# Optimization experiments

Measured on AMD Instinct MI355X. Metric: run time of the kernel, lower is better.

Reference implementation:

```python
import jax, jax.numpy as jnp
import numpy as np

HOPS = 3  # matches init kwarg hops=3


def setup_inputs() -> dict:
    key = jax.random.key(0)
    k1, k2, k3, k4 = jax.random.split(key, 4)
    B, N, D, K = 4, 8192, 128, 32
    x = jax.random.normal(k1, (B, N, D), dtype=jnp.float32)
    knn_idx = jax.random.randint(k2, (B, N, K), 0, N)
    # nn.Linear(dim, 3*dim, bias=False): y = x @ W_qkv  (W stored as (D, 3D))
    W_qkv = jax.random.normal(k3, (D, 3 * D), dtype=jnp.float32) / np.sqrt(D)
    # nn.Linear(dim, dim) with bias
    W_out = jax.random.normal(k4, (D, D), dtype=jnp.float32) / np.sqrt(D)
    b_out = jnp.zeros((D,), dtype=jnp.float32)
    return {"x": x, "knn_idx": knn_idx, "W_qkv": W_qkv, "W_out": W_out, "b_out": b_out}


def reference(x, knn_idx, W_qkv, W_out, b_out):
    B, N, D = x.shape
    K = knn_idx.shape[-1]
    qkv = x @ W_qkv                      # [B,N,3D]
    q, kf, vf = jnp.split(qkv, 3, axis=-1)
    b_ids = jnp.arange(B)[:, None, None]  # broadcast with knn_idx -> (B,N,K)
    denom = K + 1e-6

    def diffuse(f):
        # adj @ f: out[knn_idx[b,n,j]] += f[b,n]; duplicates coalesce-sum.
        return jnp.zeros_like(f).at[b_ids, knn_idx].add(f[:, :, None, :]) / denom

    for _ in range(HOPS):
        vf = diffuse(vf)
        kf = diffuse(kf)

    attn = jnp.sum(q * kf, axis=-1, keepdims=True)  # [B,N,1]
    return (attn * vf) @ W_out + b_out
```

## Files before the change

### kernel.cpp

```cpp
#include <hip/hip_runtime.h>
#include <hip/hip_fp16.h>

#define BB     4
#define NN     8192
#define DD     128
#define KNN    32
#define BN     (BB*NN)
#define NK     (NN*KNN)
#define RPB    64
#define RROWS  128
#define RCAP   4608
#define NRANGE (BB*RPB)
#define SCAP   4608
#define BCAP   48

typedef _Float16 half8 __attribute__((ext_vector_type(8)));
typedef float f32x4 __attribute__((ext_vector_type(4)));

static __device__ __forceinline__ float inv_denom() { return 1.0f / 32.000001f; }

__global__ void compute_bmat(const float* __restrict__ Wqkv,
                             const float* __restrict__ Wout,
                             _Float16* __restrict__ BT16,
                             int* __restrict__ gcursor) {
    int e = blockIdx.x;
    int j = threadIdx.x;
    if (e == 0) gcursor[j] = 0;
    float acc = 0.f;
    if (j < DD) {
        int c = j;
        #pragma unroll 4
        for (int d = 0; d < DD; ++d)
            acc += Wqkv[c*3*DD + d] * Wqkv[e*3*DD + DD + d];
    } else {
        int o = j - DD;
        #pragma unroll 4
        for (int d = 0; d < DD; ++d)
            acc += Wqkv[e*3*DD + 2*DD + d] * Wout[d*DD + o];
    }
    BT16[(size_t)j*DD + e] = (_Float16)acc;
}

__global__ __launch_bounds__(256) void cast16_kernel(const float* __restrict__ in,
                                                     __half* __restrict__ out16) {
    int t = blockIdx.x * 256 + threadIdx.x;
    const float4* p = reinterpret_cast<const float4*>(in) + (size_t)t*2;
    float4 a = p[0], b = p[1];
    uint4 w;
    w.x = __builtin_bit_cast(unsigned, __floats2half2_rn(a.x, a.y));
    w.y = __builtin_bit_cast(unsigned, __floats2half2_rn(a.z, a.w));
    w.z = __builtin_bit_cast(unsigned, __floats2half2_rn(b.x, b.y));
    w.w = __builtin_bit_cast(unsigned, __floats2half2_rn(b.z, b.w));
    *(reinterpret_cast<uint4*>(out16) + t) = w;
}

__global__ __launch_bounds__(256) void partition_kernel(
        const int* __restrict__ idx,
        int* __restrict__ staging,
        int* __restrict__ gcursor) {
    __shared__ int bucket[RPB][BCAP];
    __shared__ int bcnt[RPB];
    __shared__ int gbase[RPB];

    int t  = threadIdx.x;
    int bb = blockIdx.x;
    int batch = bb >> 8;
    int c = bb & 255;
    if (t < RPB) bcnt[t] = 0;
    __syncthreads();

    int4 v = reinterpret_cast<const int4*>(idx)[batch*(NK/4) + c*256 + t];
    int nrow = (c*256 + t) >> 3;
    int mm[4] = {v.x, v.y, v.z, v.w};
    #pragma unroll
    for (int j = 0; j < 4; ++j) {
        int m = mm[j];
        int r = m >> 7;
        int p = atomicAdd(&bcnt[r], 1);
        if (p < BCAP) bucket[r][p] = ((m & 127) << 13) | nrow;
    }
    __syncthreads();

    if (t < RPB) {
        int n = min(bcnt[t], BCAP);
        bcnt[t] = n;
        gbase[t] = atomicAdd(&gcursor[batch*RPB + t], n);
    }
    __syncthreads();

    for (int u = t; u < RPB*BCAP; u += 256) {
        int k = u / BCAP, s = u % BCAP;
        if (s < bcnt[k])
            staging[(size_t)(batch*RPB + k)*SCAP + gbase[k] + s] = bucket[k][s];
    }
}

__global__ __launch_bounds__(512) void bin_kernel(
        const int* __restrict__ staging,
        const int* __restrict__ gcursor,
        unsigned short* __restrict__ srcs16,
        int* __restrict__ meta) {
    __shared__ unsigned short binned[RCAP];
    __shared__ int hist[RROWS], pfx[RROWS], cur[RROWS];

    int t  = threadIdx.x;
    int rg = blockIdx.x;
    int cnt = gcursor[rg];
    if (cnt > SCAP) cnt = SCAP;
    const int* sp = staging + (size_t)rg*SCAP;

    if (t < RROWS) { hist[t] = 0; cur[t] = 0; }
    __syncthreads();

    for (int u = t; u < cnt; u += 512)
        atomicAdd(&hist[sp[u] >> 13], 1);
    __syncthreads();

    if (t < 64) {
        int a = hist[2*t], b = hist[2*t+1];
        int s = a + b;
        #pragma unroll
        for (int d = 1; d < 64; d <<= 1) {
            int v = __shfl_up(s, d, 64);
            if (t >= d) s += v;
        }
        int excl = s - (a + b);
        pfx[2*t]   = excl;
        pfx[2*t+1] = excl + a;
    }
    __syncthreads();

    for (int u = t; u < cnt; u += 512) {
        int e = sp[u];
        int ml = e >> 13;
        int p = atomicAdd(&cur[ml], 1);
        binned[pfx[ml] + p] = (unsigned short)(e & 8191);
    }
    __syncthreads();

    int base = rg * RCAP;
    for (int u = t; u < cnt; u += 512) srcs16[base + u] = binned[u];
    if (t < RROWS) {
        int grow = (rg >> 6)*NN + (rg & 63)*RROWS + t;
        meta[grow] = ((base + pfx[t]) << 8) | min(hist[t], 255);
    }
}

__global__ __launch_bounds__(256) void hop_kernel(
        const __half* __restrict__ fin, __half* __restrict__ fout,
        const int* __restrict__ meta,
        const unsigned short* __restrict__ srcs16) {
    int i = blockIdx.x;
    int xcd = i & 7;
    int batch = xcd >> 1;
    int j = ((i >> 3) << 1) | (xcd & 1);
    int wave = threadIdx.x >> 6;
    int lane = threadIdx.x & 63;
    int h = lane >> 4;
    int l16 = lane & 15;
    int g0 = batch*NN + j*8 + wave*2;

    int mt0 = meta[g0], mt1 = meta[g0 + 1];
    int off0 = mt0 >> 8, cnt0 = mt0 & 255;
    int off1 = mt1 >> 8, cnt1 = mt1 & 255;
    const unsigned short* sp0 = srcs16 + off0;
    const unsigned short* sp1 = srcs16 + off1;
    const __half* fbatch = fin + (size_t)batch*NN*DD;
    int laneoff = l16*8;

    int sA[8], sB[8];
    #pragma unroll
    for (int u = 0; u < 8; ++u) {
        int a = sp0[h + 4*u]; sA[u] = (a > NN-1) ? 0 : a;
        int b = sp1[h + 4*u]; sB[u] = (b > NN-1) ? 0 : b;
    }
    uint4 vA[8], vB[8];
    #pragma unroll
    for (int u = 0; u < 8; ++u)
        vA[u] = *reinterpret_cast<const uint4*>(fbatch + (size_t)sA[u]*DD + laneoff);
    #pragma unroll
    for (int u = 0; u < 8; ++u)
        vB[u] = *reinterpret_cast<const uint4*>(fbatch + (size_t)sB[u]*DD + laneoff);

    float acc0[8] = {0,0,0,0,0,0,0,0};
    float acc1[8] = {0,0,0,0,0,0,0,0};
    auto accum = [](float* acc, const uint4& v, float m) {
        float2 f0 = __half22float2(__builtin_bit_cast(__half2, v.x));
        float2 f1 = __half22float2(__builtin_bit_cast(__half2, v.y));
        float2 f2 = __half22float2(__builtin_bit_cast(__half2, v.z));
        float2 f3 = __half22float2(__builtin_bit_cast(__half2, v.w));
        acc[0] = fmaf(f0.x, m, acc[0]); acc[1] = fmaf(f0.y, m, acc[1]);
        acc[2] = fmaf(f1.x, m, acc[2]); acc[3] = fmaf(f1.y, m, acc[3]);
        acc[4] = fmaf(f2.x, m, acc[4]); acc[5] = fmaf(f2.y, m, acc[5]);
        acc[6] = fmaf(f3.x, m, acc[6]); acc[7] = fmaf(f3.y, m, acc[7]);
    };
    #pragma unroll
    for (int u = 0; u < 8; ++u) {
        accum(acc0, vA[u], (h + 4*u < cnt0) ? 1.f : 0.f);
        accum(acc1, vB[u], (h + 4*u < cnt1) ? 1.f : 0.f);
    }

    if (cnt0 > 32) {
        uint4 v2[4]; int s2[4];
        #pragma unroll
        for (int u = 0; u < 4; ++u) {
            int s = sp0[32 + h + 4*u]; s2[u] = (s > NN-1) ? 0 : s;
        }
        #pragma unroll
        for (int u = 0; u < 4; ++u)
            v2[u] = *reinterpret_cast<const uint4*>(fbatch + (size_t)s2[u]*DD + laneoff);
        #pragma unroll
        for (int u = 0; u < 4; ++u)
            accum(acc0, v2[u], (32 + h + 4*u < cnt0) ? 1.f : 0.f);
        for (int e = 48 + h; e < cnt0; e += 4) {
            int s = sp0[e];
            uint4 v = *reinterpret_cast<const uint4*>(fbatch + (size_t)s*DD + laneoff);
            accum(acc0, v, 1.f);
        }
    }
    if (cnt1 > 32) {
        uint4 v2[4]; int s2[4];
        #pragma unroll
        for (int u = 0; u < 4; ++u) {
            int s = sp1[32 + h + 4*u]; s2[u] = (s > NN-1) ? 0 : s;
        }
        #pragma unroll
        for (int u = 0; u < 4; ++u)
            v2[u] = *reinterpret_cast<const uint4*>(fbatch + (size_t)s2[u]*DD + laneoff);
        #pragma unroll
        for (int u = 0; u < 4; ++u)
            accum(acc1, v2[u], (32 + h + 4*u < cnt1) ? 1.f : 0.f);
        for (int e = 48 + h; e < cnt1; e += 4) {
            int s = sp1[e];
            uint4 v = *reinterpret_cast<const uint4*>(fbatch + (size_t)s*DD + laneoff);
            accum(acc1, v, 1.f);
        }
    }

    #pragma unroll
    for (int q = 0; q < 8; ++q) {
        acc0[q] += __shfl_xor(acc0[q], 16);
        acc0[q] += __shfl_xor(acc0[q], 32);
        acc1[q] += __shfl_xor(acc1[q], 16);
        acc1[q] += __shfl_xor(acc1[q], 32);
    }

    const float s = inv_denom();
    if (h == 0) {
        uint4 w;
        w.x = __builtin_bit_cast(unsigned, __floats2half2_rn(acc0[0]*s, acc0[1]*s));
        w.y = __builtin_bit_cast(unsigned, __floats2half2_rn(acc0[2]*s, acc0[3]*s));
        w.z = __builtin_bit_cast(unsigned, __floats2half2_rn(acc0[4]*s, acc0[5]*s));
        w.w = __builtin_bit_cast(unsigned, __floats2half2_rn(acc0[6]*s, acc0[7]*s));
        *reinterpret_cast<uint4*>(fout + (size_t)g0*DD + laneoff) = w;
    } else if (h == 1) {
        uint4 w;
        w.x = __builtin_bit_cast(unsigned, __floats2half2_rn(acc1[0]*s, acc1[1]*s));
        w.y = __builtin_bit_cast(unsigned, __floats2half2_rn(acc1[2]*s, acc1[3]*s));
        w.z = __builtin_bit_cast(unsigned, __floats2half2_rn(acc1[4]*s, acc1[5]*s));
        w.w = __builtin_bit_cast(unsigned, __floats2half2_rn(acc1[6]*s, acc1[7]*s));
        *reinterpret_cast<uint4*>(fout + (size_t)(g0+1)*DD + laneoff) = w;
    }
}

__global__ __launch_bounds__(256) void final_mfma(
        const __half* __restrict__ x3h, const float* __restrict__ x,
        const _Float16* __restrict__ BT16, const float* __restrict__ bout,
        float* __restrict__ out) {
    __shared__ float attn_l[2][16];
    int t = threadIdx.x;
    int w = t >> 6;
    int lane = t & 63;
    int role = w & 1;
    int rh = w >> 1;
    int row0 = blockIdx.x * 32 + rh * 16;
    int lr = lane & 15;
    int lg = lane >> 4;

    const _Float16* x3p = reinterpret_cast<const _Float16*>(x3h);

    half8 a[4];
    #pragma unroll
    for (int kc = 0; kc < 4; ++kc)
        a[kc] = *reinterpret_cast<const half8*>(
            x3p + (size_t)(row0 + lr)*DD + kc*32 + lg*8);

    f32x4 acc[8];
    #pragma unroll
    for (int ti = 0; ti < 8; ++ti) {
        acc[ti] = (f32x4){0.f, 0.f, 0.f, 0.f};
        int col = role*128 + ti*16 + lr;
        const _Float16* bp = BT16 + (size_t)col*DD + lg*8;
        #pragma unroll
        for (int kc = 0; kc < 4; ++kc) {
            half8 b = *reinterpret_cast<const half8*>(bp + kc*32);
            acc[ti] = __builtin_amdgcn_mfma_f32_16x16x32_f16(a[kc], b, acc[ti], 0, 0, 0);
        }
    }

    if (role == 0) {
        #pragma unroll
        for (int reg = 0; reg < 4; ++reg) {
            int row = row0 + lg*4 + reg;
            const float* xr = x + (size_t)row*DD;
            float p = 0.f;
            #pragma unroll
            for (int ti = 0; ti < 8; ++ti)
                p = fmaf(acc[ti][reg], xr[ti*16 + lr], p);
            p += __shfl_xor(p, 1); p += __shfl_xor(p, 2);
            p += __shfl_xor(p, 4); p += __shfl_xor(p, 8);
            if (lr == 0) attn_l[rh][lg*4 + reg] = p;
        }
    }
    __syncthreads();
    if (role == 1) {
        #pragma unroll
        for (int reg = 0; reg < 4; ++reg) {
            int row = row0 + lg*4 + reg;
            float at = attn_l[rh][lg*4 + reg];
            float* orow = out + (size_t)row*DD;
            #pragma unroll
            for (int ti = 0; ti < 8; ++ti) {
                int col = ti*16 + lr;
                orow[col] = fmaf(at, acc[ti][reg], bout[col]);
            }
        }
    }
}

extern "C" void kernel_launch(void* const* d_in, const int* in_sizes, int n_in,
                              void* d_out, int out_size, void* d_ws, size_t ws_size,
                              hipStream_t stream) {
    const float* x    = (const float*)d_in[0];
    const int*   idx  = (const int*)  d_in[1];
    const float* Wqkv = (const float*)d_in[2];
    const float* Wout = (const float*)d_in[3];
    const float* bout = (const float*)d_in[4];
    float* out = (float*)d_out;

    char* ws = (char*)d_ws;
    __half*         x16     = (__half*)(ws);
    __half*         fa16    = (__half*)(ws + 8388608);
    __half*         fb16    = (__half*)(ws + 16777216);
    unsigned short* srcs16  = (unsigned short*)(ws + 25165824);
    int*            meta    = (int*)(ws + 27525376);
    _Float16*       BT16    = (_Float16*)(ws + 27656448);
    int*            staging = (int*)(ws + 27787520);
    int*            gcursor = (int*)(ws + 32506112);

    compute_bmat<<<DD, 256, 0, stream>>>(Wqkv, Wout, BT16, gcursor);
    cast16_kernel<<<BN*DD/8/256, 256, 0, stream>>>(x, x16);
    partition_kernel<<<1024, 256, 0, stream>>>(idx, staging, gcursor);
    bin_kernel<<<NRANGE, 512, 0, stream>>>(staging, gcursor, srcs16, meta);

    hop_kernel<<<4096, 256, 0, stream>>>(x16,  fa16, meta, srcs16);
    hop_kernel<<<4096, 256, 0, stream>>>(fa16, fb16, meta, srcs16);
    hop_kernel<<<4096, 256, 0, stream>>>(fb16, fa16, meta, srcs16);

    final_mfma<<<BN/32, 256, 0, stream>>>(fa16, x, BT16, bout, out);
}
```

Before: 115.7 us.

## Fuse bmat, fp16 cast and partition into one prep kernel; self-reset cursor

Merges the weight-product, x-to-fp16 cast and index partition kernels into a single prep kernel, removing two launches. The global cursor moves to a device-global array that bin_kernel resets to zero after reading, so no separate zeroing step is needed. This relies on the cursor starting at zero on the first call (static device memory is zero-initialised) and on every run completing bin_kernel. The first 128 blocks also carry the matmul work, which adds load imbalance inside the fused kernel.

```diff
diff --git a/kernel.cpp b/kernel.cpp
--- a/kernel.cpp
+++ b/kernel.cpp
@@ -19,51 +19,50 @@
 
 static __device__ __forceinline__ float inv_denom() { return 1.0f / 32.000001f; }
 
-__global__ void compute_bmat(const float* __restrict__ Wqkv,
-                             const float* __restrict__ Wout,
-                             _Float16* __restrict__ BT16,
-                             int* __restrict__ gcursor) {
-    int e = blockIdx.x;
-    int j = threadIdx.x;
-    if (e == 0) gcursor[j] = 0;
-    float acc = 0.f;
-    if (j < DD) {
-        int c = j;
-        #pragma unroll 4
-        for (int d = 0; d < DD; ++d)
-            acc += Wqkv[c*3*DD + d] * Wqkv[e*3*DD + DD + d];
-    } else {
-        int o = j - DD;
-        #pragma unroll 4
-        for (int d = 0; d < DD; ++d)
-            acc += Wqkv[e*3*DD + 2*DD + d] * Wout[d*DD + o];
-    }
-    BT16[(size_t)j*DD + e] = (_Float16)acc;
-}
-
-__global__ __launch_bounds__(256) void cast16_kernel(const float* __restrict__ in,
-                                                     __half* __restrict__ out16) {
-    int t = blockIdx.x * 256 + threadIdx.x;
-    const float4* p = reinterpret_cast<const float4*>(in) + (size_t)t*2;
-    float4 a = p[0], b = p[1];
-    uint4 w;
-    w.x = __builtin_bit_cast(unsigned, __floats2half2_rn(a.x, a.y));
-    w.y = __builtin_bit_cast(unsigned, __floats2half2_rn(a.z, a.w));
-    w.z = __builtin_bit_cast(unsigned, __floats2half2_rn(b.x, b.y));
-    w.w = __builtin_bit_cast(unsigned, __floats2half2_rn(b.z, b.w));
-    *(reinterpret_cast<uint4*>(out16) + t) = w;
-}
-
-__global__ __launch_bounds__(256) void partition_kernel(
-        const int* __restrict__ idx,
-        int* __restrict__ staging,
-        int* __restrict__ gcursor) {
+__device__ int g_gcursor[NRANGE];
+
+__global__ __launch_bounds__(256) void prep_kernel(
+        const float* __restrict__ x, const int* __restrict__ idx,
+        const float* __restrict__ Wqkv, const float* __restrict__ Wout,
+        __half* __restrict__ x16, _Float16* __restrict__ BT16,
+        int* __restrict__ staging) {
     __shared__ int bucket[RPB][BCAP];
     __shared__ int bcnt[RPB];
     __shared__ int gbase[RPB];
 
     int t  = threadIdx.x;
     int bb = blockIdx.x;
+
+    #pragma unroll
+    for (int c = 0; c < 2; ++c) {
+        int tt = (bb*2 + c)*256 + t;
+        const float4* p = reinterpret_cast<const float4*>(x) + (size_t)tt*2;
+        float4 a = p[0], b = p[1];
+        uint4 w;
+        w.x = __builtin_bit_cast(unsigned, __floats2half2_rn(a.x, a.y));
+        w.y = __builtin_bit_cast(unsigned, __floats2half2_rn(a.z, a.w));
+        w.z = __builtin_bit_cast(unsigned, __floats2half2_rn(b.x, b.y));
+        w.w = __builtin_bit_cast(unsigned, __floats2half2_rn(b.z, b.w));
+        *(reinterpret_cast<uint4*>(x16) + tt) = w;
+    }
+
+    if (bb < 128) {
+        int e = bb;
+        float acc = 0.f;
+        if (t < DD) {
+            int cc = t;
+            #pragma unroll 4
+            for (int d = 0; d < DD; ++d)
+                acc += Wqkv[cc*3*DD + d] * Wqkv[e*3*DD + DD + d];
+        } else {
+            int o = t - DD;
+            #pragma unroll 4
+            for (int d = 0; d < DD; ++d)
+                acc += Wqkv[e*3*DD + 2*DD + d] * Wout[d*DD + o];
+        }
+        BT16[(size_t)t*DD + e] = (_Float16)acc;
+    }
+
     int batch = bb >> 8;
     int c = bb & 255;
     if (t < RPB) bcnt[t] = 0;
@@ -84,7 +83,7 @@
     if (t < RPB) {
         int n = min(bcnt[t], BCAP);
         bcnt[t] = n;
-        gbase[t] = atomicAdd(&gcursor[batch*RPB + t], n);
+        gbase[t] = atomicAdd(&g_gcursor[batch*RPB + t], n);
     }
     __syncthreads();
 
@@ -97,7 +96,6 @@
 
 __global__ __launch_bounds__(512) void bin_kernel(
         const int* __restrict__ staging,
-        const int* __restrict__ gcursor,
         unsigned short* __restrict__ srcs16,
         int* __restrict__ meta) {
     __shared__ unsigned short binned[RCAP];
@@ -105,7 +103,7 @@
 
     int t  = threadIdx.x;
     int rg = blockIdx.x;
-    int cnt = gcursor[rg];
+    int cnt = g_gcursor[rg];
     if (cnt > SCAP) cnt = SCAP;
     const int* sp = staging + (size_t)rg*SCAP;
 
@@ -144,6 +142,7 @@
         int grow = (rg >> 6)*NN + (rg & 63)*RROWS + t;
         meta[grow] = ((base + pfx[t]) << 8) | min(hist[t], 255);
     }
+    if (t == 0) g_gcursor[rg] = 0;
 }
 
 __global__ __launch_bounds__(256) void hop_kernel(
@@ -346,12 +345,9 @@
     int*            meta    = (int*)(ws + 27525376);
     _Float16*       BT16    = (_Float16*)(ws + 27656448);
     int*            staging = (int*)(ws + 27787520);
-    int*            gcursor = (int*)(ws + 32506112);
-
-    compute_bmat<<<DD, 256, 0, stream>>>(Wqkv, Wout, BT16, gcursor);
-    cast16_kernel<<<BN*DD/8/256, 256, 0, stream>>>(x, x16);
-    partition_kernel<<<1024, 256, 0, stream>>>(idx, staging, gcursor);
-    bin_kernel<<<NRANGE, 512, 0, stream>>>(staging, gcursor, srcs16, meta);
+
+    prep_kernel<<<1024, 256, 0, stream>>>(x, idx, Wqkv, Wout, x16, BT16, staging);
+    bin_kernel<<<NRANGE, 512, 0, stream>>>(staging, srcs16, meta);
 
     hop_kernel<<<4096, 256, 0, stream>>>(x16,  fa16, meta, srcs16);
     hop_kernel<<<4096, 256, 0, stream>>>(fa16, fb16, meta, srcs16);
```

New measurement: 112.2 us. 3.0% less time.
